# Kernel optimization log

Hardware: AMD Instinct MI355X
Metric: run time of the kernel (lower is better)

Reference implementation:

```python
import jax, jax.numpy as jnp
import numpy as np

B, N, R, C = 8, 300, 36, 256
IOU_THR, CONF_THR = 0.7, 0.3
OUT, SR = 7, 2  # roi_align output 7x7, sampling_ratio fixed to 2 (torchvision adaptive -1 approximated)


def pairwise_iou(a, b):
    area_a = (a[:, 2] - a[:, 0]) * (a[:, 3] - a[:, 1])
    area_b = (b[:, 2] - b[:, 0]) * (b[:, 3] - b[:, 1])
    lt = jnp.maximum(a[:, None, :2], b[None, :, :2])
    rb = jnp.minimum(a[:, None, 2:], b[None, :, 2:])
    wh = jnp.clip(rb - lt, 0.0)
    inter = wh[..., 0] * wh[..., 1]
    return inter / (area_a[:, None] + area_b[None, :] - inter + 1e-9)


def nms_select(boxes, scores):
    # confidence filter -> hard NMS -> keep top R in score order (fixed-shape, masked)
    s = jnp.where(scores > CONF_THR, scores, -jnp.inf)
    order = jnp.argsort(-s)
    b = boxes[order]
    v = s[order] > -jnp.inf
    iou = pairwise_iou(b, b)
    idx = jnp.arange(N)
    def body(i, keep):
        sup = keep[i] & (iou[i] > IOU_THR) & (idx > i)
        return keep & (~sup)
    keep = jax.lax.fori_loop(0, N, body, v)
    sel = jnp.argsort((~keep).astype(jnp.int32))[:R]  # stable sort: kept boxes first, score-ordered
    return b[sel], keep[sel]


def pooled_roi(feat, boxes):
    # roi_align(7x7, sampling_ratio=2, spatial_scale=1, aligned=False) followed by
    # AdaptiveAvgPool2d((1,1)) == mean of the 14x14 bilinear samples per ROI (fused here).
    _, H, W = feat.shape
    x1, y1, x2, y2 = boxes[:, 0], boxes[:, 1], boxes[:, 2], boxes[:, 3]
    rw = jnp.maximum(x2 - x1, 1.0)
    rh = jnp.maximum(y2 - y1, 1.0)
    g = (jnp.arange(OUT * SR) + 0.5) / (OUT * SR)  # sample centers in [0,1)
    Y = (y1[:, None] + rh[:, None] * g)[:, :, None]  # [R,G,1]
    X = (x1[:, None] + rw[:, None] * g)[:, None, :]  # [R,1,G]
    oob = (Y < -1.0) | (Y > H) | (X < -1.0) | (X > W)
    y = jnp.clip(Y, 0.0, H - 1)
    x = jnp.clip(X, 0.0, W - 1)
    y0 = jnp.floor(y).astype(jnp.int32)
    x0 = jnp.floor(x).astype(jnp.int32)
    y1i = jnp.minimum(y0 + 1, H - 1)
    x1i = jnp.minimum(x0 + 1, W - 1)
    ly = y - y0
    lx = x - x0
    v = (feat[:, y0, x0] * (1 - ly) * (1 - lx) + feat[:, y0, x1i] * (1 - ly) * lx
         + feat[:, y1i, x0] * ly * (1 - lx) + feat[:, y1i, x1i] * ly * lx)  # [C,R,G,G]
    v = jnp.where(oob[None], 0.0, v)
    return v.mean(axis=(2, 3)).T  # [R,C]


def setup_inputs() -> dict:
    key = jax.random.key(0)
    kc, kw, ks, k0, k1, k2, k3 = jax.random.split(key, 7)
    cxy = jax.random.uniform(kc, (B, N, 2), minval=0.0, maxval=200.0)
    wh = jax.random.uniform(kw, (B, N, 2), minval=8.0, maxval=120.0)
    boxes = jnp.concatenate([jnp.maximum(cxy - wh / 2, 0.0), cxy + wh / 2], axis=-1)
    scores = jax.random.uniform(ks, (B, N))
    feat0 = jax.random.normal(k0, (B, C, 200, 200), dtype=jnp.float32)
    feat1 = jax.random.normal(k1, (B, C, 100, 100), dtype=jnp.float32)
    feat2 = jax.random.normal(k2, (B, C, 50, 50), dtype=jnp.float32)
    feat3 = jax.random.normal(k3, (B, C, 25, 25), dtype=jnp.float32)
    return {"boxes": boxes, "scores": scores, "feat0": feat0, "feat1": feat1,
            "feat2": feat2, "feat3": feat3}


def reference(boxes, scores, feat0, feat1, feat2, feat3):
    sel_boxes, sel_valid = jax.vmap(nms_select)(boxes, scores)  # [B,R,4], [B,R]
    d = sel_boxes[..., 2:] - sel_boxes[..., :2]
    sizes = jnp.sqrt(jnp.maximum((d ** 2).sum(-1), 1e-12))
    lv = jnp.clip(jnp.floor(4.0 + jnp.log2(sizes / 224.0 * 4.0)), 2.0, 5.0).astype(jnp.int32) - 2
    out = jnp.zeros((B, R, C), boxes.dtype)
    for l, feat in enumerate([feat0, feat1, feat2, feat3]):
        pooled = jax.vmap(pooled_roi)(feat, sel_boxes)  # [B,R,C]
        mask = (lv == l) & sel_valid
        out = jnp.where(mask[..., None], pooled, out)
    return out  # [B, top_rois, 256]; rows for invalid ROIs are zero
```

## Files before the change

kernel.cpp:

```cpp
#include <hip/hip_runtime.h>
#include <math.h>

#define BB   8
#define NB   300
#define RSEL 36
#define NCH  256
#define NW   10
#define IOU_THR  0.7f
#define CONF_THR 0.3f


__global__ __launch_bounds__(256) void nms_kernel(
    const float* __restrict__ boxes, const float* __restrict__ scores,
    float* __restrict__ ws)
{
    const int b   = blockIdx.x;
    const int tid = threadIdx.x;

    __shared__ float ss[NB];
    __shared__ float sbx[NB][4];
    __shared__ float ssv[NB];
    __shared__ unsigned int supp[NB][NW];
    __shared__ unsigned int keepw[NW];
    __shared__ int kept_total;

    const float NEG_INF = -__builtin_inff();

    for (int i = tid; i < NB; i += blockDim.x) {
        float sc = scores[b * NB + i];
        ss[i] = (sc > CONF_THR) ? sc : NEG_INF;
    }
    for (int t = tid; t < NB * NW; t += blockDim.x)
        ((unsigned int*)supp)[t] = 0u;
    if (tid < NW) keepw[tid] = 0u;
    __syncthreads();

    for (int i = tid; i < NB; i += blockDim.x) {
        float si = ss[i];
        int r = 0;
        for (int j = 0; j < NB; ++j) {
            float sj = ss[j];
            r += (sj > si) || (sj == si && j < i);
        }
        ssv[r]    = si;
        sbx[r][0] = boxes[(b * NB + i) * 4 + 0];
        sbx[r][1] = boxes[(b * NB + i) * 4 + 1];
        sbx[r][2] = boxes[(b * NB + i) * 4 + 2];
        sbx[r][3] = boxes[(b * NB + i) * 4 + 3];
        if (si > NEG_INF) atomicOr(&keepw[r >> 5], 1u << (r & 31));
    }
    __syncthreads();

    for (int t = tid; t < NB * NB; t += blockDim.x) {
        int i = t / NB, j = t % NB;
        if (j <= i) continue;
        float ax1 = sbx[i][0], ay1 = sbx[i][1], ax2 = sbx[i][2], ay2 = sbx[i][3];
        float bx1 = sbx[j][0], by1 = sbx[j][1], bx2 = sbx[j][2], by2 = sbx[j][3];
        float area_a = (ax2 - ax1) * (ay2 - ay1);
        float area_b = (bx2 - bx1) * (by2 - by1);
        float ltx = fmaxf(ax1, bx1), lty = fmaxf(ay1, by1);
        float rbx = fminf(ax2, bx2), rby = fminf(ay2, by2);
        float wx = fmaxf(rbx - ltx, 0.0f), wy = fmaxf(rby - lty, 0.0f);
        float inter = wx * wy;
        float iou = inter / (area_a + area_b - inter + 1e-9f);
        if (iou > IOU_THR) atomicOr(&supp[i][j >> 5], 1u << (j & 31));
    }
    __syncthreads();

    if (tid == 0) {
        unsigned int kp[NW];
#pragma unroll
        for (int k = 0; k < NW; ++k) kp[k] = keepw[k];
        for (int i = 0; i < NB; ++i) {
            if ((kp[i >> 5] >> (i & 31)) & 1u) {
#pragma unroll
                for (int k = 0; k < NW; ++k) kp[k] &= ~supp[i][k];
            }
        }
        int tot = 0;
#pragma unroll
        for (int k = 0; k < NW; ++k) { keepw[k] = kp[k]; tot += __popc(kp[k]); }
        kept_total = tot;
    }
    __syncthreads();

    for (int i = tid; i < NB; i += blockDim.x) {
        int w = i >> 5, bt = i & 31;
        int kbit = (keepw[w] >> bt) & 1;
        int pre_kept = 0;
        for (int k = 0; k < w; ++k) pre_kept += __popc(keepw[k]);
        pre_kept += __popc(keepw[w] & ((1u << bt) - 1u));
        int pos = kbit ? pre_kept : (kept_total + (i - pre_kept));
        if (pos < RSEL) {
            float x1 = sbx[i][0], y1 = sbx[i][1], x2 = sbx[i][2], y2 = sbx[i][3];
            float dx = x2 - x1, dy = y2 - y1;
            float sz = sqrtf(fmaxf(dx * dx + dy * dy, 1e-12f));
            float l  = floorf(4.0f + log2f((sz / 224.0f) * 4.0f));
            l = fminf(fmaxf(l, 2.0f), 5.0f) - 2.0f;
            float* o = ws + (size_t)(b * RSEL + pos) * 8;
            o[0] = x1; o[1] = y1; o[2] = x2; o[3] = y2;
            o[4] = l;  o[5] = (float)kbit;
        }
    }
}

__global__ __launch_bounds__(256) void pool_kernel(
    const float* __restrict__ f0, const float* __restrict__ f1,
    const float* __restrict__ f2, const float* __restrict__ f3,
    const float* __restrict__ ws, float* __restrict__ out)
{
    const int blk = blockIdx.x;
    const int b   = blk / RSEL;
    const int r   = blk % RSEL;
    const int tid = threadIdx.x;

    const float* wsr = ws + (size_t)(b * RSEL + r) * 8;
    float x1 = wsr[0], y1 = wsr[1], x2 = wsr[2], y2 = wsr[3];
    int   lv = (int)wsr[4];
    int   valid = wsr[5] > 0.5f;

    size_t oidx = ((size_t)(b * RSEL + r)) * NCH + tid;
    if (!valid) { out[oidx] = 0.0f; return; }

    const float* feat; int H;
    if      (lv == 0) { feat = f0; H = 200; }
    else if (lv == 1) { feat = f1; H = 100; }
    else if (lv == 2) { feat = f2; H = 50;  }
    else              { feat = f3; H = 25;  }
    const int W = H;

    __shared__ int   iy0[14], iy1[14], ix0[14], ix1[14];
    __shared__ float fly[14], flx[14];
    __shared__ int   oy[14], ox[14];

    if (tid < 28) {
        int k = (tid < 14) ? tid : tid - 14;
        float g = (k + 0.5f) * (1.0f / 14.0f);
        if (tid < 14) {
            float rh = fmaxf(y2 - y1, 1.0f);
            float Y  = y1 + rh * g;
            oy[k] = (Y < -1.0f) || (Y > (float)H);
            float y = fminf(fmaxf(Y, 0.0f), (float)(H - 1));
            int y0 = (int)floorf(y);
            iy0[k] = y0;
            iy1[k] = min(y0 + 1, H - 1);
            fly[k] = y - (float)y0;
        } else {
            float rw = fmaxf(x2 - x1, 1.0f);
            float X  = x1 + rw * g;
            ox[k] = (X < -1.0f) || (X > (float)W);
            float x = fminf(fmaxf(X, 0.0f), (float)(W - 1));
            int x0 = (int)floorf(x);
            ix0[k] = x0;
            ix1[k] = min(x0 + 1, W - 1);
            flx[k] = x - (float)x0;
        }
    }
    __syncthreads();

    const float* fc = feat + ((size_t)b * NCH + tid) * (size_t)(H * W);
    float acc = 0.0f;
    for (int i = 0; i < 14; ++i) {
        if (oy[i]) continue;
        const float* r0 = fc + iy0[i] * W;
        const float* r1 = fc + iy1[i] * W;
        float wy = fly[i];
        for (int j = 0; j < 14; ++j) {
            if (ox[j]) continue;
            float wx = flx[j];
            float v00 = r0[ix0[j]], v01 = r0[ix1[j]];
            float v10 = r1[ix0[j]], v11 = r1[ix1[j]];
            float top = v00 + wx * (v01 - v00);
            float bot = v10 + wx * (v11 - v10);
            acc += top + wy * (bot - top);
        }
    }
    out[oidx] = acc * (1.0f / 196.0f);
}

extern "C" void kernel_launch(void* const* d_in, const int* in_sizes, int n_in,
                              void* d_out, int out_size, void* d_ws, size_t ws_size,
                              hipStream_t stream) {
    const float* boxes  = (const float*)d_in[0];
    const float* scores = (const float*)d_in[1];
    const float* f0     = (const float*)d_in[2];
    const float* f1     = (const float*)d_in[3];
    const float* f2     = (const float*)d_in[4];
    const float* f3     = (const float*)d_in[5];
    float* ws  = (float*)d_ws;
    float* out = (float*)d_out;

    nms_kernel<<<BB, 256, 0, stream>>>(boxes, scores, ws);
    pool_kernel<<<BB * RSEL, 256, 0, stream>>>(f0, f1, f2, f3, ws, out);
}
```

Measured before the change: 634.6 us.

## Factor bilinear ROI pooling into separable row and column weights with coalesced loads

The NMS kernel now precomputes, for each selected ROI, deduplicated row indices with summed y-weights and a contiguous column window with summed x-weights, and writes them to workspace. The pool kernel splits channels across a second grid dimension. Each wave reads contiguous feature rows across its lanes, accumulates row-weighted sums for 16 channels, then applies the x-weight and reduces across lanes. This replaces per-thread scattered 4-tap gathers with coalesced row loads and fewer redundant reads. The cost is extra serial setup work in the NMS tail, and a column window capped at 64 that would drop contributions for wider ROIs.

```diff
diff --git a/kernel.cpp b/kernel.cpp
--- a/kernel.cpp
+++ b/kernel.cpp
@@ -8,6 +8,7 @@
 #define NW   10
 #define IOU_THR  0.7f
 #define CONF_THR 0.3f
+#define WSTR 128
 
 
 __global__ __launch_bounds__(256) void nms_kernel(
@@ -19,7 +20,6 @@
 
     __shared__ float ss[NB];
     __shared__ float sbx[NB][4];
-    __shared__ float ssv[NB];
     __shared__ unsigned int supp[NB][NW];
     __shared__ unsigned int keepw[NW];
     __shared__ int kept_total;
@@ -42,7 +42,6 @@
             float sj = ss[j];
             r += (sj > si) || (sj == si && j < i);
         }
-        ssv[r]    = si;
         sbx[r][0] = boxes[(b * NB + i) * 4 + 0];
         sbx[r][1] = boxes[(b * NB + i) * 4 + 1];
         sbx[r][2] = boxes[(b * NB + i) * 4 + 2];
@@ -91,15 +90,84 @@
         for (int k = 0; k < w; ++k) pre_kept += __popc(keepw[k]);
         pre_kept += __popc(keepw[w] & ((1u << bt) - 1u));
         int pos = kbit ? pre_kept : (kept_total + (i - pre_kept));
-        if (pos < RSEL) {
-            float x1 = sbx[i][0], y1 = sbx[i][1], x2 = sbx[i][2], y2 = sbx[i][3];
-            float dx = x2 - x1, dy = y2 - y1;
-            float sz = sqrtf(fmaxf(dx * dx + dy * dy, 1e-12f));
-            float l  = floorf(4.0f + log2f((sz / 224.0f) * 4.0f));
-            l = fminf(fmaxf(l, 2.0f), 5.0f) - 2.0f;
-            float* o = ws + (size_t)(b * RSEL + pos) * 8;
-            o[0] = x1; o[1] = y1; o[2] = x2; o[3] = y2;
-            o[4] = l;  o[5] = (float)kbit;
+        if (pos >= RSEL) continue;
+
+        float* o = ws + (size_t)(b * RSEL + pos) * WSTR;
+        for (int k = 0; k < WSTR; ++k) o[k] = 0.0f;
+        if (!kbit) continue;
+
+        float bx1 = sbx[i][0], by1 = sbx[i][1], bx2 = sbx[i][2], by2 = sbx[i][3];
+        float dx = bx2 - bx1, dy = by2 - by1;
+        float sz = sqrtf(fmaxf(dx * dx + dy * dy, 1e-12f));
+        float l  = floorf(4.0f + log2f(sz * (4.0f / 224.0f)));
+        l = fminf(fmaxf(l, 2.0f), 5.0f) - 2.0f;
+        int lvl = (int)l;
+        int H = (lvl == 0) ? 200 : ((lvl == 1) ? 100 : ((lvl == 2) ? 50 : 25));
+        float Hf = (float)H;
+
+        o[0] = 1.0f;
+        o[1] = l;
+
+        int ridx[28]; float rwt[28]; int nr = 0;
+        float rh = fmaxf(dy, 1.0f);
+        for (int s = 0; s < 14; ++s) {
+            float g = (s + 0.5f) * (1.0f / 14.0f);
+            float Y = by1 + rh * g;
+            bool oob = (Y < -1.0f) || (Y > Hf);
+            float yc = fminf(fmaxf(Y, 0.0f), Hf - 1.0f);
+            int y0 = (int)floorf(yc);
+            int y1i = min(y0 + 1, H - 1);
+            float ly = yc - (float)y0;
+            float w0 = oob ? 0.0f : (1.0f - ly);
+            float w1 = oob ? 0.0f : ly;
+            if (w0 != 0.0f) {
+                int m = 0; for (; m < nr; ++m) if (ridx[m] == y0) break;
+                if (m == nr) { ridx[nr] = y0; rwt[nr] = w0; ++nr; } else rwt[m] += w0;
+            }
+            if (w1 != 0.0f) {
+                int m = 0; for (; m < nr; ++m) if (ridx[m] == y1i) break;
+                if (m == nr) { ridx[nr] = y1i; rwt[nr] = w1; ++nr; } else rwt[m] += w1;
+            }
+        }
+        o[2] = (float)nr;
+        for (int m = 0; m < nr; ++m) {
+            o[8 + m]  = (float)ridx[m];
+            o[36 + m] = rwt[m] * (1.0f / 196.0f);
+        }
+
+        float rw = fmaxf(dx, 1.0f);
+        int xmn = 1 << 30, xmx = -1;
+        for (int s = 0; s < 14; ++s) {
+            float g = (s + 0.5f) * (1.0f / 14.0f);
+            float X = bx1 + rw * g;
+            bool oob = (X < -1.0f) || (X > Hf);
+            if (oob) continue;
+            float xc = fminf(fmaxf(X, 0.0f), Hf - 1.0f);
+            int x0 = (int)floorf(xc);
+            int x1i = min(x0 + 1, H - 1);
+            float lx = xc - (float)x0;
+            if ((1.0f - lx) != 0.0f) { xmn = min(xmn, x0);  xmx = max(xmx, x0);  }
+            if (lx != 0.0f)          { xmn = min(xmn, x1i); xmx = max(xmx, x1i); }
+        }
+        int ce = (xmx >= xmn) ? (xmx - xmn + 1) : 0;
+        if (ce > 64) ce = 64;
+        o[3] = (float)ce;
+        o[4] = (float)xmn;
+
+        if (ce > 0) {
+            for (int s = 0; s < 14; ++s) {
+                float g = (s + 0.5f) * (1.0f / 14.0f);
+                float X = bx1 + rw * g;
+                bool oob = (X < -1.0f) || (X > Hf);
+                if (oob) continue;
+                float xc = fminf(fmaxf(X, 0.0f), Hf - 1.0f);
+                int x0 = (int)floorf(xc);
+                int x1i = min(x0 + 1, H - 1);
+                float lx = xc - (float)x0;
+                float w0 = 1.0f - lx;
+                if (w0 != 0.0f) { int p = x0 - xmn;  if (p >= 0 && p < 64) o[64 + p] += w0; }
+                if (lx != 0.0f) { int p = x1i - xmn; if (p >= 0 && p < 64) o[64 + p] += lx; }
+            }
         }
     }
 }
@@ -109,73 +177,64 @@
     const float* __restrict__ f2, const float* __restrict__ f3,
     const float* __restrict__ ws, float* __restrict__ out)
 {
-    const int blk = blockIdx.x;
-    const int b   = blk / RSEL;
-    const int r   = blk % RSEL;
-    const int tid = threadIdx.x;
-
-    const float* wsr = ws + (size_t)(b * RSEL + r) * 8;
-    float x1 = wsr[0], y1 = wsr[1], x2 = wsr[2], y2 = wsr[3];
-    int   lv = (int)wsr[4];
-    int   valid = wsr[5] > 0.5f;
-
-    size_t oidx = ((size_t)(b * RSEL + r)) * NCH + tid;
-    if (!valid) { out[oidx] = 0.0f; return; }
+    const int br   = blockIdx.x;
+    const int cg   = blockIdx.y;
+    const int b    = br / RSEL;
+    const int tid  = threadIdx.x;
+    const int lane = tid & 63;
+    const int wv   = tid >> 6;
+
+    __shared__ float smeta[WSTR];
+    for (int t = tid; t < WSTR; t += 256) smeta[t] = ws[(size_t)br * WSTR + t];
+    __syncthreads();
+
+    const size_t obase = (size_t)br * NCH + (size_t)cg * 64;
+    if (smeta[0] == 0.0f) {
+        if (tid < 64) out[obase + tid] = 0.0f;
+        return;
+    }
+
+    const int lvl = (int)smeta[1];
+    const int nr  = (int)smeta[2];
+    const int ce  = (int)smeta[3];
+    const int xmn = (int)smeta[4];
 
     const float* feat; int H;
-    if      (lv == 0) { feat = f0; H = 200; }
-    else if (lv == 1) { feat = f1; H = 100; }
-    else if (lv == 2) { feat = f2; H = 50;  }
-    else              { feat = f3; H = 25;  }
+    if      (lvl == 0) { feat = f0; H = 200; }
+    else if (lvl == 1) { feat = f1; H = 100; }
+    else if (lvl == 2) { feat = f2; H = 50;  }
+    else               { feat = f3; H = 25;  }
     const int W = H;
-
-    __shared__ int   iy0[14], iy1[14], ix0[14], ix1[14];
-    __shared__ float fly[14], flx[14];
-    __shared__ int   oy[14], ox[14];
-
-    if (tid < 28) {
-        int k = (tid < 14) ? tid : tid - 14;
-        float g = (k + 0.5f) * (1.0f / 14.0f);
-        if (tid < 14) {
-            float rh = fmaxf(y2 - y1, 1.0f);
-            float Y  = y1 + rh * g;
-            oy[k] = (Y < -1.0f) || (Y > (float)H);
-            float y = fminf(fmaxf(Y, 0.0f), (float)(H - 1));
-            int y0 = (int)floorf(y);
-            iy0[k] = y0;
-            iy1[k] = min(y0 + 1, H - 1);
-            fly[k] = y - (float)y0;
-        } else {
-            float rw = fmaxf(x2 - x1, 1.0f);
-            float X  = x1 + rw * g;
-            ox[k] = (X < -1.0f) || (X > (float)W);
-            float x = fminf(fmaxf(X, 0.0f), (float)(W - 1));
-            int x0 = (int)floorf(x);
-            ix0[k] = x0;
-            ix1[k] = min(x0 + 1, W - 1);
-            flx[k] = x - (float)x0;
-        }
-    }
-    __syncthreads();
-
-    const float* fc = feat + ((size_t)b * NCH + tid) * (size_t)(H * W);
-    float acc = 0.0f;
-    for (int i = 0; i < 14; ++i) {
-        if (oy[i]) continue;
-        const float* r0 = fc + iy0[i] * W;
-        const float* r1 = fc + iy1[i] * W;
-        float wy = fly[i];
-        for (int j = 0; j < 14; ++j) {
-            if (ox[j]) continue;
-            float wx = flx[j];
-            float v00 = r0[ix0[j]], v01 = r0[ix1[j]];
-            float v10 = r1[ix0[j]], v11 = r1[ix1[j]];
-            float top = v00 + wx * (v01 - v00);
-            float bot = v10 + wx * (v11 - v10);
-            acc += top + wy * (bot - top);
-        }
-    }
-    out[oidx] = acc * (1.0f / 196.0f);
+    const size_t cstr = (size_t)H * W;
+
+    const bool  ld  = (lane < ce);
+    const float wxl = ld ? smeta[64 + lane] : 0.0f;
+
+    const int c0 = cg * 64 + wv * 16;
+    const float* fb = feat + ((size_t)b * NCH + c0) * cstr + xmn + lane;
+
+    float acc[16];
+#pragma unroll
+    for (int u = 0; u < 16; ++u) acc[u] = 0.0f;
+
+    for (int r = 0; r < nr; ++r) {
+        int   row = (int)smeta[8 + r];
+        float rwt = smeta[36 + r];
+        const float* p = fb + (size_t)row * W;
+#pragma unroll
+        for (int u = 0; u < 16; ++u) {
+            float v = 0.0f;
+            if (ld) v = p[u * cstr];
+            acc[u] = fmaf(rwt, v, acc[u]);
+        }
+    }
+
+#pragma unroll
+    for (int u = 0; u < 16; ++u) {
+        float a = acc[u] * wxl;
+        for (int off = 32; off; off >>= 1) a += __shfl_xor(a, off, 64);
+        if (lane == 0) out[obase + wv * 16 + u] = a;
+    }
 }
 
 extern "C" void kernel_launch(void* const* d_in, const int* in_sizes, int n_in,
@@ -191,5 +250,6 @@
     float* out = (float*)d_out;
 
     nms_kernel<<<BB, 256, 0, stream>>>(boxes, scores, ws);
-    pool_kernel<<<BB * RSEL, 256, 0, stream>>>(f0, f1, f2, f3, ws, out);
+    dim3 pgrid(BB * RSEL, 4);
+    pool_kernel<<<pgrid, 256, 0, stream>>>(f0, f1, f2, f3, ws, out);
 }
```

New measurement: 564.7 us. -11.0%, faster.
